# Optimization experiments

Hardware: AMD Instinct MI355X
Metric: run time of the kernel (lower is better)

## Reference

```python
import jax, jax.numpy as jnp
import numpy as np

B, L, T, TE, H = 16, 100, 50, 100, 200  # batch, post_len, triples/token, t_embed, hidden
NEG_INF = jnp.float32(-1e30)


def setup_inputs() -> dict:
    key = jax.random.key(0)
    ks = jax.random.split(key, 9)
    sc = 0.1
    inp = {
        'head_emb': jax.random.normal(ks[0], (B, L, T, TE), jnp.float32),
        'rel_emb':  jax.random.normal(ks[1], (B, L, T, TE), jnp.float32),
        'tail_emb': jax.random.normal(ks[2], (B, L, T, TE), jnp.float32),
        'Wh_w': jax.random.normal(ks[3], (H, TE), jnp.float32) * sc,
        'Wh_b': jax.random.normal(ks[4], (H,), jnp.float32) * sc,
        'Wr_w': jax.random.normal(ks[5], (H, TE), jnp.float32) * sc,
        'Wr_b': jax.random.normal(ks[6], (H,), jnp.float32) * sc,
        'Wt_w': jax.random.normal(ks[7], (H, TE), jnp.float32) * sc,
        'Wt_b': jax.random.normal(ks[8], (H,), jnp.float32) * sc,
    }
    # structured padding masks (like PAD_IDX padding): last quarter of triples padded,
    # last 10 post positions padded. Every unpadded post position has valid triples.
    inp['triple_mask'] = jnp.broadcast_to(jnp.arange(T) >= (3 * T) // 4, (B, L, T))
    inp['post_mask'] = jnp.broadcast_to(jnp.arange(L) >= L - 10, (B, L))
    return inp


def reference(head_emb, rel_emb, tail_emb, Wh_w, Wh_b, Wr_w, Wr_b, Wt_w, Wt_b,
              triple_mask, post_mask):
    # Linear projections: [B,L,T,TE] @ [TE,H] -> [B,L,T,H]
    h = jnp.einsum('bltd,hd->blth', head_emb, Wh_w) + Wh_b
    r = jnp.einsum('bltd,hd->blth', rel_emb, Wr_w) + Wr_b
    t = jnp.einsum('bltd,hd->blth', tail_emb, Wt_w) + Wt_b
    # triple-wise additive attention logit: [B,L,T]
    static_logit = jnp.sum(r * jnp.tanh(h + t), axis=-1)
    static_logit = jnp.where(triple_mask, NEG_INF, static_logit)
    static_logit = jnp.where(post_mask[:, :, None], 0.0, static_logit)
    static_attn = jax.nn.softmax(static_logit, axis=-1)  # [B,L,T]
    # weighted entity aggregation: ent = cat(head, tail) -> [B,L,2*TE]
    ent = jnp.concatenate([head_emb, tail_emb], axis=-1)
    static_graph = jnp.einsum('blte,blt->ble', ent, static_attn)
    return static_graph
```

## Files before the change

### kernel.cpp

```cpp
#include <hip/hip_runtime.h>
#include <math.h>

#define BB 16
#define LL 100
#define TT 50
#define TE 100
#define HH 200
#define NTL 13
#define NEG_INF_F (-1e30f)

typedef _Float16 fp16;
typedef fp16 half8 __attribute__((ext_vector_type(8)));
typedef float f32x4 __attribute__((ext_vector_type(4)));

#define MFMA16 __builtin_amdgcn_mfma_f32_16x16x32_f16

__global__ __launch_bounds__(256)
void wprep_kernel(const float* __restrict__ Wh, const float* __restrict__ Wr,
                  const float* __restrict__ Wt,
                  const float* __restrict__ Bh, const float* __restrict__ Br,
                  const float* __restrict__ Bt,
                  fp16* __restrict__ WB) {
    int idx = blockIdx.x * 256 + threadIdx.x;
    int elem = idx & 7;
    int lane = (idx >> 3) & 63;
    int ks   = (idx >> 9) & 3;
    int np   = idx >> 11;
    int p    = np % 3;
    int nt   = np / 3;
    int k = ks * 32 + 8 * (lane >> 4) + elem;
    int n = nt * 16 + (lane & 15);
    const float* W  = (p == 0) ? Wh : (p == 1) ? Wr : Wt;
    const float* Bi = (p == 0) ? Bh : (p == 1) ? Br : Bt;
    float v = 0.0f;
    if (n < HH) {
        if (k < TE)       v = W[n * TE + k];
        else if (k == TE) v = Bi[n];
    }
    WB[idx] = (fp16)v;
}

#define GATHER1(SRC, DST, RV)                                                   \
    {                                                                           \
        _Pragma("unroll")                                                       \
        for (int ks_ = 0; ks_ < 4; ++ks_) {                                     \
            f32x4 v0 = {0.f, 0.f, 0.f, 0.f}, v1 = {0.f, 0.f, 0.f, 0.f};         \
            float one_ = 0.f;                                                   \
            if (ks_ < 3) {                                                      \
                const int d0 = ks_ * 32 + 8 * lg;                               \
                if (RV) {                                                       \
                    v0 = *(const f32x4*)((SRC) + d0);                           \
                    v1 = *(const f32x4*)((SRC) + d0 + 4);                       \
                }                                                               \
            } else if ((RV) && lg == 0) {                                       \
                v0 = *(const f32x4*)((SRC) + 96);                               \
                one_ = 1.0f;                                                    \
            }                                                                   \
            half8 h8;                                                           \
            _Pragma("unroll")                                                   \
            for (int i_ = 0; i_ < 4; ++i_) {                                    \
                h8[i_]     = (fp16)v0[i_];                                      \
                h8[4 + i_] = (fp16)v1[i_];                                      \
            }                                                                   \
            if (ks_ == 3) h8[4] = (fp16)one_;            \
            DST[ks_] = h8;                                                      \
        }                                                                       \
    }

#define STAGE3(GBASE, LBASE)                                                    \
    {                                                                           \
        _Pragma("unroll")                                                       \
        for (int u_ = 0; u_ < 3; ++u_) {                                        \
            const int unit_ = wv * 3 + u_;                                      \
            __builtin_amdgcn_global_load_lds(                                   \
                (const __attribute__((address_space(1))) unsigned int*)         \
                    ((GBASE) + unit_ * 512 + l * 8),                            \
                (__attribute__((address_space(3))) unsigned int*)               \
                    ((LBASE) + unit_ * 512),                                    \
                16, 0, 0);                                                      \
        }                                                                       \
    }

__global__ __launch_bounds__(256, 3)
void ccm_mfma_kernel(const float* __restrict__ head, const float* __restrict__ rel,
                     const float* __restrict__ tail,
                     const fp16* __restrict__ WB,
                     const int* __restrict__ tmask, const int* __restrict__ pmask,
                     float* __restrict__ out) {
    __shared__ fp16 sw[2][6144];
    __shared__ float sscore[2][64];
    __shared__ float sattn[2][64];

    const int tid = threadIdx.x;
    const int wv  = tid >> 6;
    const int l   = tid & 63;
    const int lr  = l & 15;
    const int lg  = l >> 4;
    const int blx = wv >> 1;
    const int wp  = wv & 1;
    const int bl  = 2 * blockIdx.x + blx;
    const int r0  = wp * 32 + lr;
    const int r1  = wp * 32 + 16 + lr;
    const bool rv0 = r0 < TT;
    const bool rv1 = r1 < TT;
    const size_t base0 = (size_t)bl * TT * TE;

    half8 H0[4], R0[4], T0[4], H1[4], R1[4], T1[4];
    GATHER1(head + base0 + (size_t)r0 * TE, H0, rv0);
    GATHER1(rel  + base0 + (size_t)r0 * TE, R0, rv0);
    GATHER1(tail + base0 + (size_t)r0 * TE, T0, rv0);
    GATHER1(head + base0 + (size_t)r1 * TE, H1, rv1);
    GATHER1(rel  + base0 + (size_t)r1 * TE, R1, rv1);
    GATHER1(tail + base0 + (size_t)r1 * TE, T1, rv1);

    STAGE3(WB, &sw[0][0]);

    float sc0[4] = {0.f, 0.f, 0.f, 0.f};
    float sc1[4] = {0.f, 0.f, 0.f, 0.f};

    #pragma unroll 1
    for (int nt = 0; nt < NTL; ++nt) {
        const int cur = nt & 1;
        if (nt + 1 < NTL) {
            STAGE3(WB + (size_t)(nt + 1) * 6144, &sw[cur ^ 1][0]);
            __builtin_amdgcn_sched_barrier(0);
            asm volatile("s_waitcnt vmcnt(3)" ::: "memory");
        } else {
            __builtin_amdgcn_sched_barrier(0);
            asm volatile("s_waitcnt vmcnt(0)" ::: "memory");
        }
        __syncthreads();

        const fp16* wbuf = (const fp16*)&sw[cur][0];
        f32x4 aH0 = {0,0,0,0}, aR0 = {0,0,0,0}, aT0 = {0,0,0,0};
        f32x4 aH1 = {0,0,0,0}, aR1 = {0,0,0,0}, aT1 = {0,0,0,0};
        #pragma unroll
        for (int ks = 0; ks < 4; ++ks) {
            half8 wH = *(const half8*)(wbuf + (0 * 4 + ks) * 512 + l * 8);
            half8 wR = *(const half8*)(wbuf + (1 * 4 + ks) * 512 + l * 8);
            half8 wT = *(const half8*)(wbuf + (2 * 4 + ks) * 512 + l * 8);
            aH0 = MFMA16(H0[ks], wH, aH0, 0, 0, 0);
            aH1 = MFMA16(H1[ks], wH, aH1, 0, 0, 0);
            aR0 = MFMA16(R0[ks], wR, aR0, 0, 0, 0);
            aR1 = MFMA16(R1[ks], wR, aR1, 0, 0, 0);
            aT0 = MFMA16(T0[ks], wT, aT0, 0, 0, 0);
            aT1 = MFMA16(T1[ks], wT, aT1, 0, 0, 0);
        }
        #pragma unroll
        for (int g = 0; g < 4; ++g) {
            float s0 = aH0[g] + aT0[g];
            float e0 = __expf(2.f * s0);
            float t0 = 1.f - 2.f / (e0 + 1.f);
            sc0[g] = fmaf(aR0[g], t0, sc0[g]);
            float s1 = aH1[g] + aT1[g];
            float e1 = __expf(2.f * s1);
            float t1 = 1.f - 2.f / (e1 + 1.f);
            sc1[g] = fmaf(aR1[g], t1, sc1[g]);
        }
        __syncthreads();
    }

    #pragma unroll
    for (int g = 0; g < 4; ++g) {
        float s = sc0[g];
        s += __shfl_xor(s, 1); s += __shfl_xor(s, 2);
        s += __shfl_xor(s, 4); s += __shfl_xor(s, 8);
        const int tr = wp * 32 + lg * 4 + g;
        if (lr == 0 && tr < TT) sscore[blx][tr] = s;
        float s1 = sc1[g];
        s1 += __shfl_xor(s1, 1); s1 += __shfl_xor(s1, 2);
        s1 += __shfl_xor(s1, 4); s1 += __shfl_xor(s1, 8);
        const int tr1 = wp * 32 + 16 + lg * 4 + g;
        if (lr == 0 && tr1 < TT) sscore[blx][tr1] = s1;
    }
    __syncthreads();

    if (tid < 128) {
        const int bx = tid >> 6;
        const int t  = tid & 63;
        const int mybl = 2 * blockIdx.x + bx;
        const bool valid = t < TT;
        float lgt = valid ? sscore[bx][t] : 0.f;
        const bool tm = valid ? (tmask[mybl * TT + t] != 0) : false;
        const bool pm = pmask[mybl] != 0;
        float logit = pm ? 0.f : (tm ? NEG_INF_F : lgt);
        float mx = valid ? logit : -3.0e38f;
        #pragma unroll
        for (int o = 32; o; o >>= 1) mx = fmaxf(mx, __shfl_xor(mx, o));
        float e = valid ? __expf(logit - mx) : 0.f;
        float s = e;
        #pragma unroll
        for (int o = 32; o; o >>= 1) s += __shfl_xor(s, o);
        if (valid) sattn[bx][t] = e / s;
    }
    __syncthreads();

    #pragma unroll
    for (int it = 0; it < 2; ++it) {
        const int i = tid + it * 256;
        if (i < 2 * (2 * TE)) {
            const int bx = (i >= 2 * TE) ? 1 : 0;
            const int e  = i - bx * (2 * TE);
            const size_t b2 = (size_t)(2 * blockIdx.x + bx) * TT * TE;
            const float* src = (e < TE) ? head + b2 + e : tail + b2 + (e - TE);
            float acc = 0.f;
            #pragma unroll
            for (int t = 0; t < TT; ++t) acc = fmaf(src[t * TE], sattn[bx][t], acc);
            out[(size_t)(2 * blockIdx.x + bx) * (2 * TE) + e] = acc;
        }
    }
}

extern "C" void kernel_launch(void* const* d_in, const int* in_sizes, int n_in,
                              void* d_out, int out_size, void* d_ws, size_t ws_size,
                              hipStream_t stream) {
    const float* head = (const float*)d_in[0];
    const float* rel  = (const float*)d_in[1];
    const float* tail = (const float*)d_in[2];
    const float* Whw  = (const float*)d_in[3];
    const float* Whb  = (const float*)d_in[4];
    const float* Wrw  = (const float*)d_in[5];
    const float* Wrb  = (const float*)d_in[6];
    const float* Wtw  = (const float*)d_in[7];
    const float* Wtb  = (const float*)d_in[8];
    const int* tmask  = (const int*)d_in[9];
    const int* pmask  = (const int*)d_in[10];
    float* out = (float*)d_out;

    fp16* WB = (fp16*)d_ws;

    wprep_kernel<<<(NTL * 3 * 2048) / 256, 256, 0, stream>>>(Whw, Wrw, Wtw,
                                                             Whb, Wrb, Wtb, WB);
    ccm_mfma_kernel<<<(BB * LL) / 2, 256, 0, stream>>>(head, rel, tail, WB,
                                                       tmask, pmask, out);
}
```

Before: 179.0 us.

## Fuse weight prep and attention into one persistent kernel with grid barriers

```diff
diff --git a/kernel.cpp b/kernel.cpp
--- a/kernel.cpp
+++ b/kernel.cpp
@@ -7,6 +7,8 @@
 #define TE 100
 #define HH 200
 #define NTL 13
+#define NBLK 1250
+#define NWPREP (NTL * 3 * 2048)
 #define NEG_INF_F (-1e30f)
 
 typedef _Float16 fp16;
@@ -15,32 +17,7 @@
 
 #define MFMA16 __builtin_amdgcn_mfma_f32_16x16x32_f16
 
-__global__ __launch_bounds__(256)
-void wprep_kernel(const float* __restrict__ Wh, const float* __restrict__ Wr,
-                  const float* __restrict__ Wt,
-                  const float* __restrict__ Bh, const float* __restrict__ Br,
-                  const float* __restrict__ Bt,
-                  fp16* __restrict__ WB) {
-    int idx = blockIdx.x * 256 + threadIdx.x;
-    int elem = idx & 7;
-    int lane = (idx >> 3) & 63;
-    int ks   = (idx >> 9) & 3;
-    int np   = idx >> 11;
-    int p    = np % 3;
-    int nt   = np / 3;
-    int k = ks * 32 + 8 * (lane >> 4) + elem;
-    int n = nt * 16 + (lane & 15);
-    const float* W  = (p == 0) ? Wh : (p == 1) ? Wr : Wt;
-    const float* Bi = (p == 0) ? Bh : (p == 1) ? Br : Bt;
-    float v = 0.0f;
-    if (n < HH) {
-        if (k < TE)       v = W[n * TE + k];
-        else if (k == TE) v = Bi[n];
-    }
-    WB[idx] = (fp16)v;
-}
-
-#define GATHER1(SRC, DST, RV)                                                   \
+#define GATHER1(SRC, DST)                                                       \
     {                                                                           \
         _Pragma("unroll")                                                       \
         for (int ks_ = 0; ks_ < 4; ++ks_) {                                     \
@@ -48,11 +25,9 @@
             float one_ = 0.f;                                                   \
             if (ks_ < 3) {                                                      \
                 const int d0 = ks_ * 32 + 8 * lg;                               \
-                if (RV) {                                                       \
-                    v0 = *(const f32x4*)((SRC) + d0);                           \
-                    v1 = *(const f32x4*)((SRC) + d0 + 4);                       \
-                }                                                               \
-            } else if ((RV) && lg == 0) {                                       \
+                v0 = *(const f32x4*)((SRC) + d0);                               \
+                v1 = *(const f32x4*)((SRC) + d0 + 4);                           \
+            } else if (lg == 0) {                                               \
                 v0 = *(const f32x4*)((SRC) + 96);                               \
                 one_ = 1.0f;                                                    \
             }                                                                   \
@@ -81,133 +56,151 @@
         }                                                                       \
     }
 
-__global__ __launch_bounds__(256, 3)
-void ccm_mfma_kernel(const float* __restrict__ head, const float* __restrict__ rel,
-                     const float* __restrict__ tail,
-                     const fp16* __restrict__ WB,
-                     const int* __restrict__ tmask, const int* __restrict__ pmask,
-                     float* __restrict__ out) {
+__device__ __forceinline__ void grid_barrier(unsigned* bar, int k) {
+    __syncthreads();
+    if (threadIdx.x == 0) {
+        __threadfence();
+        __hip_atomic_fetch_add(&bar[k], 1u, __ATOMIC_ACQ_REL,
+                               __HIP_MEMORY_SCOPE_AGENT);
+        unsigned tries = 0;
+        while (__hip_atomic_load(&bar[k], __ATOMIC_RELAXED,
+                                 __HIP_MEMORY_SCOPE_AGENT) < (unsigned)NBLK) {
+            __builtin_amdgcn_s_sleep(16);
+            if (++tries > 4000000u) break;
+        }
+        __threadfence();
+    }
+    __syncthreads();
+}
+
+__global__ __launch_bounds__(256, 5)
+void ccm_fused_kernel(const float* __restrict__ head, const float* __restrict__ rel,
+                      const float* __restrict__ tail,
+                      const float* __restrict__ Whw, const float* __restrict__ Whb,
+                      const float* __restrict__ Wrw, const float* __restrict__ Wrb,
+                      const float* __restrict__ Wtw, const float* __restrict__ Wtb,
+                      const int* __restrict__ tmask, const int* __restrict__ pmask,
+                      float* __restrict__ out,
+                      unsigned* __restrict__ bar,
+                      fp16* __restrict__ WB,
+                      float* __restrict__ score) {
     __shared__ fp16 sw[2][6144];
-    __shared__ float sscore[2][64];
-    __shared__ float sattn[2][64];
+    __shared__ float sattn[64];
 
     const int tid = threadIdx.x;
     const int wv  = tid >> 6;
     const int l   = tid & 63;
     const int lr  = l & 15;
     const int lg  = l >> 4;
-    const int blx = wv >> 1;
-    const int wp  = wv & 1;
-    const int bl  = 2 * blockIdx.x + blx;
-    const int r0  = wp * 32 + lr;
-    const int r1  = wp * 32 + 16 + lr;
-    const bool rv0 = r0 < TT;
-    const bool rv1 = r1 < TT;
-    const size_t base0 = (size_t)bl * TT * TE;
-
-    half8 H0[4], R0[4], T0[4], H1[4], R1[4], T1[4];
-    GATHER1(head + base0 + (size_t)r0 * TE, H0, rv0);
-    GATHER1(rel  + base0 + (size_t)r0 * TE, R0, rv0);
-    GATHER1(tail + base0 + (size_t)r0 * TE, T0, rv0);
-    GATHER1(head + base0 + (size_t)r1 * TE, H1, rv1);
-    GATHER1(rel  + base0 + (size_t)r1 * TE, R1, rv1);
-    GATHER1(tail + base0 + (size_t)r1 * TE, T1, rv1);
-
-    STAGE3(WB, &sw[0][0]);
-
-    float sc0[4] = {0.f, 0.f, 0.f, 0.f};
-    float sc1[4] = {0.f, 0.f, 0.f, 0.f};
-
-    #pragma unroll 1
-    for (int nt = 0; nt < NTL; ++nt) {
-        const int cur = nt & 1;
-        if (nt + 1 < NTL) {
-            STAGE3(WB + (size_t)(nt + 1) * 6144, &sw[cur ^ 1][0]);
-            __builtin_amdgcn_sched_barrier(0);
-            asm volatile("s_waitcnt vmcnt(3)" ::: "memory");
-        } else {
-            __builtin_amdgcn_sched_barrier(0);
-            asm volatile("s_waitcnt vmcnt(0)" ::: "memory");
-        }
-        __syncthreads();
-
-        const fp16* wbuf = (const fp16*)&sw[cur][0];
-        f32x4 aH0 = {0,0,0,0}, aR0 = {0,0,0,0}, aT0 = {0,0,0,0};
-        f32x4 aH1 = {0,0,0,0}, aR1 = {0,0,0,0}, aT1 = {0,0,0,0};
-        #pragma unroll
-        for (int ks = 0; ks < 4; ++ks) {
-            half8 wH = *(const half8*)(wbuf + (0 * 4 + ks) * 512 + l * 8);
-            half8 wR = *(const half8*)(wbuf + (1 * 4 + ks) * 512 + l * 8);
-            half8 wT = *(const half8*)(wbuf + (2 * 4 + ks) * 512 + l * 8);
-            aH0 = MFMA16(H0[ks], wH, aH0, 0, 0, 0);
-            aH1 = MFMA16(H1[ks], wH, aH1, 0, 0, 0);
-            aR0 = MFMA16(R0[ks], wR, aR0, 0, 0, 0);
-            aR1 = MFMA16(R1[ks], wR, aR1, 0, 0, 0);
-            aT0 = MFMA16(T0[ks], wT, aT0, 0, 0, 0);
-            aT1 = MFMA16(T1[ks], wT, aT1, 0, 0, 0);
-        }
+
+    {
+        const int idx = blockIdx.x * 256 + tid;
+        if (idx < NWPREP) {
+            const int elem = idx & 7;
+            const int lane = (idx >> 3) & 63;
+            const int ks   = (idx >> 9) & 3;
+            const int np   = idx >> 11;
+            const int p    = np % 3;
+            const int nt   = np / 3;
+            const int k = ks * 32 + 8 * (lane >> 4) + elem;
+            const int n = nt * 16 + (lane & 15);
+            const float* W  = (p == 0) ? Whw : (p == 1) ? Wrw : Wtw;
+            const float* Bi = (p == 0) ? Whb : (p == 1) ? Wrb : Wtb;
+            float v = 0.0f;
+            if (n < HH) {
+                if (k < TE)       v = W[n * TE + k];
+                else if (k == TE) v = Bi[n];
+            }
+            WB[idx] = (fp16)v;
+        }
+    }
+    grid_barrier(bar, 0);
+
+    {
+        const int wtile = blockIdx.x * 4 + wv;
+        const size_t abase = ((size_t)wtile * 16 + lr) * TE;
+
+        half8 HA[4], RA[4], TA[4];
+        GATHER1(head + abase, HA);
+        GATHER1(rel  + abase, RA);
+        GATHER1(tail + abase, TA);
+
+        STAGE3(WB, &sw[0][0]);
+
+        float sc[4] = {0.f, 0.f, 0.f, 0.f};
+
+        #pragma unroll 1
+        for (int nt = 0; nt < NTL; ++nt) {
+            const int cur = nt & 1;
+            if (nt + 1 < NTL) {
+                STAGE3(WB + (size_t)(nt + 1) * 6144, &sw[cur ^ 1][0]);
+                __builtin_amdgcn_sched_barrier(0);
+                asm volatile("s_waitcnt vmcnt(3)" ::: "memory");
+            } else {
+                __builtin_amdgcn_sched_barrier(0);
+                asm volatile("s_waitcnt vmcnt(0)" ::: "memory");
+            }
+            __syncthreads();
+
+            const fp16* wbuf = (const fp16*)&sw[cur][0];
+            f32x4 aH = {0,0,0,0}, aR = {0,0,0,0}, aT = {0,0,0,0};
+            #pragma unroll
+            for (int ks = 0; ks < 4; ++ks) {
+                half8 wH = *(const half8*)(wbuf + (0 * 4 + ks) * 512 + l * 8);
+                half8 wR = *(const half8*)(wbuf + (1 * 4 + ks) * 512 + l * 8);
+                half8 wT = *(const half8*)(wbuf + (2 * 4 + ks) * 512 + l * 8);
+                aH = MFMA16(HA[ks], wH, aH, 0, 0, 0);
+                aR = MFMA16(RA[ks], wR, aR, 0, 0, 0);
+                aT = MFMA16(TA[ks], wT, aT, 0, 0, 0);
+            }
+            #pragma unroll
+            for (int g = 0; g < 4; ++g) {
+                float s0 = aH[g] + aT[g];
+                float e0 = __expf(2.f * s0);
+                float t0 = 1.f - 2.f / (e0 + 1.f);
+                sc[g] = fmaf(aR[g], t0, sc[g]);
+            }
+            __syncthreads();
+        }
+
         #pragma unroll
         for (int g = 0; g < 4; ++g) {
-            float s0 = aH0[g] + aT0[g];
-            float e0 = __expf(2.f * s0);
-            float t0 = 1.f - 2.f / (e0 + 1.f);
-            sc0[g] = fmaf(aR0[g], t0, sc0[g]);
-            float s1 = aH1[g] + aT1[g];
-            float e1 = __expf(2.f * s1);
-            float t1 = 1.f - 2.f / (e1 + 1.f);
-            sc1[g] = fmaf(aR1[g], t1, sc1[g]);
+            float s = sc[g];
+            s += __shfl_xor(s, 1); s += __shfl_xor(s, 2);
+            s += __shfl_xor(s, 4); s += __shfl_xor(s, 8);
+            if (lr == 0) score[wtile * 16 + lg * 4 + g] = s;
+        }
+    }
+    grid_barrier(bar, 1);
+
+    for (int mybl = blockIdx.x; mybl < BB * LL; mybl += NBLK) {
+        if (tid < 64) {
+            const int t = tid;
+            const bool valid = t < TT;
+            float lgt = valid ? score[mybl * TT + t] : 0.f;
+            const bool tm = valid ? (tmask[mybl * TT + t] != 0) : false;
+            const bool pm = pmask[mybl] != 0;
+            float logit = pm ? 0.f : (tm ? NEG_INF_F : lgt);
+            float mx = valid ? logit : -3.0e38f;
+            #pragma unroll
+            for (int o = 32; o; o >>= 1) mx = fmaxf(mx, __shfl_xor(mx, o));
+            float e = valid ? __expf(logit - mx) : 0.f;
+            float s = e;
+            #pragma unroll
+            for (int o = 32; o; o >>= 1) s += __shfl_xor(s, o);
+            if (valid) sattn[t] = e / s;
         }
         __syncthreads();
-    }
-
-    #pragma unroll
-    for (int g = 0; g < 4; ++g) {
-        float s = sc0[g];
-        s += __shfl_xor(s, 1); s += __shfl_xor(s, 2);
-        s += __shfl_xor(s, 4); s += __shfl_xor(s, 8);
-        const int tr = wp * 32 + lg * 4 + g;
-        if (lr == 0 && tr < TT) sscore[blx][tr] = s;
-        float s1 = sc1[g];
-        s1 += __shfl_xor(s1, 1); s1 += __shfl_xor(s1, 2);
-        s1 += __shfl_xor(s1, 4); s1 += __shfl_xor(s1, 8);
-        const int tr1 = wp * 32 + 16 + lg * 4 + g;
-        if (lr == 0 && tr1 < TT) sscore[blx][tr1] = s1;
-    }
-    __syncthreads();
-
-    if (tid < 128) {
-        const int bx = tid >> 6;
-        const int t  = tid & 63;
-        const int mybl = 2 * blockIdx.x + bx;
-        const bool valid = t < TT;
-        float lgt = valid ? sscore[bx][t] : 0.f;
-        const bool tm = valid ? (tmask[mybl * TT + t] != 0) : false;
-        const bool pm = pmask[mybl] != 0;
-        float logit = pm ? 0.f : (tm ? NEG_INF_F : lgt);
-        float mx = valid ? logit : -3.0e38f;
-        #pragma unroll
-        for (int o = 32; o; o >>= 1) mx = fmaxf(mx, __shfl_xor(mx, o));
-        float e = valid ? __expf(logit - mx) : 0.f;
-        float s = e;
-        #pragma unroll
-        for (int o = 32; o; o >>= 1) s += __shfl_xor(s, o);
-        if (valid) sattn[bx][t] = e / s;
-    }
-    __syncthreads();
-
-    #pragma unroll
-    for (int it = 0; it < 2; ++it) {
-        const int i = tid + it * 256;
-        if (i < 2 * (2 * TE)) {
-            const int bx = (i >= 2 * TE) ? 1 : 0;
-            const int e  = i - bx * (2 * TE);
-            const size_t b2 = (size_t)(2 * blockIdx.x + bx) * TT * TE;
-            const float* src = (e < TE) ? head + b2 + e : tail + b2 + (e - TE);
+        if (tid < 2 * TE) {
+            const size_t b2 = (size_t)mybl * TT * TE;
+            const float* src = (tid < TE) ? head + b2 + tid
+                                          : tail + b2 + (tid - TE);
             float acc = 0.f;
             #pragma unroll
-            for (int t = 0; t < TT; ++t) acc = fmaf(src[t * TE], sattn[bx][t], acc);
-            out[(size_t)(2 * blockIdx.x + bx) * (2 * TE) + e] = acc;
-        }
+            for (int t = 0; t < TT; ++t) acc = fmaf(src[t * TE], sattn[t], acc);
+            out[(size_t)mybl * (2 * TE) + tid] = acc;
+        }
+        __syncthreads();
     }
 }
 
@@ -227,10 +220,13 @@
     const int* pmask  = (const int*)d_in[10];
     float* out = (float*)d_out;
 
-    fp16* WB = (fp16*)d_ws;
-
-    wprep_kernel<<<(NTL * 3 * 2048) / 256, 256, 0, stream>>>(Whw, Wrw, Wtw,
-                                                             Whb, Wrb, Wtb, WB);
-    ccm_mfma_kernel<<<(BB * LL) / 2, 256, 0, stream>>>(head, rel, tail, WB,
-                                                       tmask, pmask, out);
+    unsigned* bar = (unsigned*)d_ws;
+    fp16* WB      = (fp16*)((char*)d_ws + 256);
+    float* score  = (float*)((char*)d_ws + 256 + NWPREP * sizeof(fp16));
+
+    hipMemsetAsync(d_ws, 0, 256, stream);
+    ccm_fused_kernel<<<NBLK, 256, 0, stream>>>(head, rel, tail,
+                                               Whw, Whb, Wrw, Wrb, Wtw, Wtb,
+                                               tmask, pmask, out,
+                                               bar, WB, score);
 }
```

Result: slower. 462.4 us (+158.4%).
